# Performance work log

Measured on AMD Instinct MI355X. Metric: run time of the kernel, lower is better.

## Reference

```python
import jax, jax.numpy as jnp
import numpy as np

D_MODEL = 1024
IDX_DIM = 64
SEQ = 4096
D_STATE = 64
EXPAND = 1
HEADDIM = 32
D_CONV = 4
D_INNER = EXPAND * D_MODEL
NHEADS = D_INNER // HEADDIM
CONV_DIM = D_INNER + 2 * D_STATE
D_IN_PROJ = 2 * D_INNER + 2 * D_STATE + NHEADS  # z, xBC, dt


def setup_inputs() -> dict:
    key = jax.random.key(0)
    ks = jax.random.split(key, 8)
    def rn(k, shape, scale=1.0):
        return jax.random.normal(k, shape, jnp.float32) * scale
    return {
        "x": rn(ks[0], (SEQ, D_MODEL)),
        "W_in": rn(ks[1], (D_IN_PROJ, D_MODEL), D_MODEL ** -0.5),
        "conv_w": rn(ks[2], (CONV_DIM, D_CONV), D_CONV ** -0.5),
        "conv_b": jnp.zeros((CONV_DIM,), jnp.float32),
        "dt_bias": rn(ks[3], (NHEADS,)),
        "A_log": jnp.log(jnp.arange(1, NHEADS + 1, dtype=jnp.float32)),
        "D": jnp.ones((NHEADS,), jnp.float32),
        "norm_w": jnp.ones((D_INNER,), jnp.float32),
        "W_out": rn(ks[4], (D_MODEL, D_INNER), D_INNER ** -0.5),
        "W_q": rn(ks[5], (IDX_DIM, D_MODEL), D_MODEL ** -0.5),
        "W_k": rn(ks[6], (IDX_DIM, D_MODEL), D_MODEL ** -0.5),
    }


def _silu(v):
    return v * jax.nn.sigmoid(v)


def _mamba2(x, W_in, conv_w, conv_b, dt_bias, A_log, Dp, norm_w, W_out):
    L = x.shape[0]
    zxbcdt = x @ W_in.T  # [L, D_IN_PROJ]
    z, xBC, dt = jnp.split(zxbcdt, [D_INNER, D_INNER + CONV_DIM], axis=-1)
    # depthwise causal conv1d, kernel D_CONV
    xc = jax.lax.conv_general_dilated(
        xBC.T[None],               # [1, C, L]
        conv_w[:, None, :],        # [C, 1, K]
        (1,), [(D_CONV - 1, 0)], feature_group_count=CONV_DIM)[0].T
    xBC = _silu(xc + conv_b)
    xs, B, C = jnp.split(xBC, [D_INNER, D_INNER + D_STATE], axis=-1)
    xs = xs.reshape(L, NHEADS, HEADDIM)
    dt = jax.nn.softplus(dt + dt_bias)   # [L, H]
    A = -jnp.exp(A_log)                  # [H]

    def step(h, inp):
        x_t, B_t, C_t, dt_t = inp        # [H,P], [N], [N], [H]
        dA = jnp.exp(dt_t * A)           # [H]
        h = h * dA[:, None, None] + (dt_t[:, None] * x_t)[:, :, None] * B_t[None, None, :]
        return h, jnp.einsum('hpn,n->hp', h, C_t)

    h0 = jnp.zeros((NHEADS, HEADDIM, D_STATE), x.dtype)
    _, ys = jax.lax.scan(step, h0, (xs, B, C, dt))  # ys: [L, H, P]
    y = ys + Dp[None, :, None] * xs
    y = y.reshape(L, D_INNER)
    y = y * _silu(z)                                 # gated RMSNorm
    y = y * jax.lax.rsqrt(jnp.mean(y * y, axis=-1, keepdims=True) + 1e-5) * norm_w
    return y @ W_out.T


def reference(x, W_in, conv_w, conv_b, dt_bias, A_log, D, norm_w, W_out, W_q, W_k):
    L = x.shape[0]
    x_mamba = _mamba2(x, W_in, conv_w, conv_b, dt_bias, A_log, D, norm_w, W_out)
    q = x_mamba @ W_q.T                  # [L, IDX_DIM]
    k = x @ W_k.T                        # [L, IDX_DIM]
    scores = jnp.einsum('ti,si->ts', q, k) * (IDX_DIM ** -0.5)
    mask = jnp.tril(jnp.ones((L, L), dtype=bool))
    return jnp.where(mask, scores, -jnp.inf)
```

## Files before the change

kernel.cpp:

```cpp
#include <hip/hip_runtime.h>
#include <math.h>

#define L_SEQ 4096
#define DMODEL 1024
#define DINNER 1024
#define DSTATE 64
#define NH 32
#define HD 32
#define CONVD 1152
#define DPROJ2 2272
#define KOFF 2208
#define QC 128
#define NC 32

#define NEG_FILL (-1e30f)

typedef __attribute__((ext_vector_type(8))) short short8;
typedef __attribute__((ext_vector_type(4))) float f32x4;
typedef unsigned short u16;

__device__ __forceinline__ u16 f2bf(float f) {
  unsigned int u = __float_as_uint(f);
  unsigned int r = (u + 0x7fffu + ((u >> 16) & 1u)) >> 16;
  return (u16)r;
}
__device__ __forceinline__ float bf2f(u16 b) {
  unsigned int u = ((unsigned int)b) << 16;
  return __uint_as_float(u);
}
__device__ __forceinline__ short8 pack8(float4 a, float4 b) {
  short8 v;
  v[0] = (short)f2bf(a.x); v[1] = (short)f2bf(a.y);
  v[2] = (short)f2bf(a.z); v[3] = (short)f2bf(a.w);
  v[4] = (short)f2bf(b.x); v[5] = (short)f2bf(b.y);
  v[6] = (short)f2bf(b.z); v[7] = (short)f2bf(b.w);
  return v;
}

__device__ __forceinline__ void g2l16(const void* g, void* l) {
  __builtin_amdgcn_global_load_lds(
      (const __attribute__((address_space(1))) unsigned int*)g,
      (__attribute__((address_space(3))) unsigned int*)l, 16, 0, 0);
}

#define CAST_N0 (L_SEQ * DMODEL / 8)
#define CAST_N1 (2208 * DMODEL / 8)
#define CAST_N2 (64 * DMODEL / 8)
#define CAST_TOTAL (CAST_N0 + CAST_N1 + 2 * CAST_N2)
#define CAST_BLKS (CAST_TOTAL / 256)
__global__ __launch_bounds__(256) void cast_tr_k(const float* __restrict__ x,
                                                 const float* __restrict__ W_in,
                                                 const float* __restrict__ W_k,
                                                 const float* __restrict__ W_q,
                                                 const float* __restrict__ W_out,
                                                 u16* __restrict__ x_bf,
                                                 u16* __restrict__ Wcat,
                                                 u16* __restrict__ Wq_bf,
                                                 u16* __restrict__ WoutT) {
  __shared__ float tile[64][65];
  int bid = blockIdx.x;
  if (bid < CAST_BLKS) {
    int gid = bid * 256 + threadIdx.x;
    const float* src;
    u16* dst;
    int i;
    if (gid < CAST_N0) { src = x; dst = x_bf; i = gid; }
    else if (gid < CAST_N0 + CAST_N1) { src = W_in; dst = Wcat; i = gid - CAST_N0; }
    else if (gid < CAST_N0 + CAST_N1 + CAST_N2) {
      src = W_k; dst = Wcat + (size_t)2208 * DMODEL; i = gid - CAST_N0 - CAST_N1;
    } else { src = W_q; dst = Wq_bf; i = gid - CAST_N0 - CAST_N1 - CAST_N2; }
    i *= 8;
    float4 f0 = *(const float4*)(src + i);
    float4 f1 = *(const float4*)(src + i + 4);
    *(short8*)(dst + i) = pack8(f0, f1);
    return;
  }
  bid -= CAST_BLKS;
  int bx = bid & 15, by = bid >> 4;
  int tx = threadIdx.x & 63, ty = threadIdx.x >> 6;
#pragma unroll
  for (int k = 0; k < 16; k++) {
    int r = ty + k * 4;
    tile[r][tx] = W_out[(size_t)(by * 64 + r) * 1024 + bx * 64 + tx];
  }
  __syncthreads();
#pragma unroll
  for (int k = 0; k < 16; k++) {
    int r = ty + k * 4;
    WoutT[(size_t)(bx * 64 + r) * 1024 + by * 64 + tx] = f2bf(tile[tx][r]);
  }
}

__global__ __launch_bounds__(256) void wqo_k(const u16* __restrict__ Wq,
                                             const u16* __restrict__ WoutT,
                                             u16* __restrict__ Wqo) {
  const int tid = threadIdx.x;
  const int wave = tid >> 6, lane = tid & 63;
  const int l15 = lane & 15, quad = lane >> 4;
  const int j0 = blockIdx.x * 64;
  f32x4 acc[4] = {};
  for (int kk = 0; kk < 32; kk++) {
    short8 b = *(const short8*)(WoutT + (size_t)(j0 + wave * 16 + l15) * 1024 + kk * 32 + quad * 8);
#pragma unroll
    for (int mi = 0; mi < 4; mi++) {
      short8 a = *(const short8*)(Wq + (size_t)(mi * 16 + l15) * 1024 + kk * 32 + quad * 8);
      acc[mi] = __builtin_amdgcn_mfma_f32_16x16x32_bf16(a, b, acc[mi], 0, 0, 0);
    }
  }
#pragma unroll
  for (int mi = 0; mi < 4; mi++)
#pragma unroll
    for (int r = 0; r < 4; r++) {
      int i = mi * 16 + quad * 4 + r;
      Wqo[(size_t)i * 1024 + j0 + wave * 16 + l15] = f2bf(acc[mi][r]);
    }
}

__global__ __launch_bounds__(256) void gemm128(const u16* __restrict__ A,
                                               const u16* __restrict__ B,
                                               u16* __restrict__ Cbf,
                                               int M, int N, int K) {
  __shared__ u16 As[128 * 32];
  __shared__ u16 Bs[128 * 32];
  const int tid = threadIdx.x;
  const int wave = tid >> 6, lane = tid & 63;
  const int m0 = blockIdx.x * 128, n0 = blockIdx.y * 128;
  const int wm = (wave >> 1) * 64, wn = (wave & 1) * 64;
  const int l15 = lane & 15, quad = lane >> 4;

  const u16* aptr[2];
  const u16* bptr[2];
  char *ldsA[2], *ldsB[2];
#pragma unroll
  for (int b = 0; b < 2; b++) {
    int ch = b * 256 + tid;
    int row = ch >> 2, q = (ch & 3) ^ ((row >> 1) & 3);
    aptr[b] = A + (size_t)(m0 + row) * K + q * 8;
    int bn = min(n0 + row, N - 1);
    bptr[b] = B + (size_t)bn * K + q * 8;
    ldsA[b] = (char*)As + b * 4096 + wave * 1024;
    ldsB[b] = (char*)Bs + b * 4096 + wave * 1024;
  }

  int offA[4], offB[4];
#pragma unroll
  for (int i = 0; i < 4; i++) {
    int ra = wm + i * 16 + l15;
    offA[i] = ra * 32 + (quad ^ ((ra >> 1) & 3)) * 8;
    int rb = wn + i * 16 + l15;
    offB[i] = rb * 32 + (quad ^ ((rb >> 1) & 3)) * 8;
  }

  f32x4 acc[4][4] = {};
  for (int k0 = 0; k0 < K; k0 += 32) {
#pragma unroll
    for (int b = 0; b < 2; b++) g2l16(aptr[b] + k0, ldsA[b]);
#pragma unroll
    for (int b = 0; b < 2; b++) g2l16(bptr[b] + k0, ldsB[b]);
    __builtin_amdgcn_s_waitcnt(0);
    __syncthreads();
    short8 af[4], bfr[4];
#pragma unroll
    for (int i = 0; i < 4; i++) af[i] = *(const short8*)(As + offA[i]);
#pragma unroll
    for (int j = 0; j < 4; j++) bfr[j] = *(const short8*)(Bs + offB[j]);
#pragma unroll
    for (int mi = 0; mi < 4; mi++)
#pragma unroll
      for (int ni = 0; ni < 4; ni++)
        acc[mi][ni] = __builtin_amdgcn_mfma_f32_16x16x32_bf16(af[mi], bfr[ni],
                                                              acc[mi][ni], 0, 0, 0);
    __syncthreads();
  }
#pragma unroll
  for (int mi = 0; mi < 4; mi++)
#pragma unroll
    for (int r = 0; r < 4; r++) {
      int grow = m0 + wm + mi * 16 + quad * 4 + r;
#pragma unroll
      for (int ni = 0; ni < 4; ni++) {
        int gcol = n0 + wn + ni * 16 + l15;
        if (gcol < N) Cbf[(size_t)grow * N + gcol] = f2bf(acc[mi][ni][r]);
      }
    }
}

__global__ __launch_bounds__(256) void splitk64(const u16* __restrict__ A,
                                                const u16* __restrict__ B,
                                                float* __restrict__ P,
                                                int M, int K) {
  __shared__ u16 As[128 * 32];
  __shared__ u16 Bs[64 * 32];
  const int tid = threadIdx.x;
  const int wave = tid >> 6, lane = tid & 63;
  const int m0 = blockIdx.x * 128;
  const int ks = blockIdx.y;
  const int wm = (wave >> 1) * 64, wn = (wave & 1) * 32;
  const int l15 = lane & 15, quad = lane >> 4;

  const int c0 = tid, c1 = 256 + tid;
  const int r0 = c0 >> 2, q0 = (c0 & 3) ^ ((r0 >> 1) & 3);
  const int r1 = c1 >> 2, q1 = (c1 & 3) ^ ((r1 >> 1) & 3);
  const int rb = tid >> 2, qb = (tid & 3) ^ ((rb >> 1) & 3);
  const u16* a0 = A + (size_t)(m0 + r0) * K + q0 * 8;
  const u16* a1 = A + (size_t)(m0 + r1) * K + q1 * 8;
  const u16* bptr = B + (size_t)rb * K + qb * 8;
  char* ldsA0 = (char*)As + wave * 1024;
  char* ldsA1 = (char*)As + 4096 + wave * 1024;
  char* ldsB = (char*)Bs + wave * 1024;

  int offA[4], offB[2];
#pragma unroll
  for (int i = 0; i < 4; i++) {
    int ra = wm + i * 16 + l15;
    offA[i] = ra * 32 + (quad ^ ((ra >> 1) & 3)) * 8;
  }
#pragma unroll
  for (int j = 0; j < 2; j++) {
    int rr = wn + j * 16 + l15;
    offB[j] = rr * 32 + (quad ^ ((rr >> 1) & 3)) * 8;
  }

  f32x4 acc[4][2] = {};
  const int kbeg = ks * 128;
  for (int k0 = kbeg; k0 < kbeg + 128; k0 += 32) {
    g2l16(a0 + k0, ldsA0);
    g2l16(a1 + k0, ldsA1);
    g2l16(bptr + k0, ldsB);
    __builtin_amdgcn_s_waitcnt(0);
    __syncthreads();
    short8 af[4], bfr[2];
#pragma unroll
    for (int i = 0; i < 4; i++) af[i] = *(const short8*)(As + offA[i]);
#pragma unroll
    for (int j = 0; j < 2; j++) bfr[j] = *(const short8*)(Bs + offB[j]);
#pragma unroll
    for (int mi = 0; mi < 4; mi++)
#pragma unroll
      for (int ni = 0; ni < 2; ni++)
        acc[mi][ni] = __builtin_amdgcn_mfma_f32_16x16x32_bf16(af[mi], bfr[ni],
                                                              acc[mi][ni], 0, 0, 0);
    __syncthreads();
  }
  float* Pp = P + (size_t)ks * M * 64;
#pragma unroll
  for (int mi = 0; mi < 4; mi++)
#pragma unroll
    for (int r = 0; r < 4; r++) {
      int grow = m0 + wm + mi * 16 + quad * 4 + r;
#pragma unroll
      for (int ni = 0; ni < 2; ni++)
        Pp[(size_t)grow * 64 + wn + ni * 16 + l15] = acc[mi][ni][r];
    }
}

__global__ __launch_bounds__(256) void reduce8_k(const float* __restrict__ P,
                                                 u16* __restrict__ out, int n) {
  int i = blockIdx.x * 256 + threadIdx.x;
  if (i >= n) return;
  float s = 0.f;
#pragma unroll
  for (int ks = 0; ks < 8; ks++) s += P[(size_t)ks * n + i];
  out[i] = f2bf(s);
}

#define CONV_BLKS (L_SEQ * 144 / 256)
__global__ __launch_bounds__(256) void conv_dt_k(const u16* __restrict__ zx,
                                                 const float* __restrict__ cw,
                                                 const float* __restrict__ cb,
                                                 u16* __restrict__ xbc,
                                                 const float* __restrict__ dt_bias,
                                                 const float* __restrict__ A_log,
                                                 float* __restrict__ dtsp,
                                                 float* __restrict__ aL) {
  if (blockIdx.x < CONV_BLKS) {
    int gid = blockIdx.x * 256 + threadIdx.x;
    int t = gid / 144;
    int c0 = (gid - t * 144) * 8;
    float acc[8];
#pragma unroll
    for (int j = 0; j < 8; j++) acc[j] = cb[c0 + j];
    float wv[8][4];
#pragma unroll
    for (int j = 0; j < 8; j++) {
      float4 w4 = *(const float4*)(cw + (c0 + j) * 4);
      wv[j][0] = w4.x; wv[j][1] = w4.y; wv[j][2] = w4.z; wv[j][3] = w4.w;
    }
#pragma unroll
    for (int k = 0; k < 4; k++) {
      int s = t - 3 + k;
      if (s >= 0) {
        short8 v = *(const short8*)(zx + (size_t)s * DPROJ2 + DINNER + c0);
#pragma unroll
        for (int j = 0; j < 8; j++) acc[j] += bf2f((u16)v[j]) * wv[j][k];
      }
    }
    short8 o;
#pragma unroll
    for (int j = 0; j < 8; j++) o[j] = (short)f2bf(acc[j] / (1.f + expf(-acc[j])));
    *(short8*)(xbc + (size_t)t * CONVD + c0) = o;
    return;
  }
  int w = threadIdx.x >> 6, lane = threadIdx.x & 63;
  int idx = (blockIdx.x - CONV_BLKS) * 4 + w;
  int h = idx & 31, c = idx >> 5;
  float negA = -expf(A_log[h]);
  float bias = dt_bias[h];
  float carry = 0.f;
#pragma unroll
  for (int seg = 0; seg < 2; seg++) {
    int t = c * QC + seg * 64 + lane;
    float xv = bf2f(zx[(size_t)t * DPROJ2 + 2176 + h]) + bias;
    float sp = (xv > 20.f) ? xv : log1pf(expf(xv));
    dtsp[(size_t)t * 32 + h] = sp;
    float v = sp * negA;
#pragma unroll
    for (int off = 1; off < 64; off <<= 1) {
      float u = __shfl_up(v, off, 64);
      if (lane >= off) v += u;
    }
    aL[(size_t)t * 32 + h] = carry + v;
    carry += __shfl(v, 63, 64);
  }
}

__global__ __launch_bounds__(256) void csg_k(const u16* __restrict__ xbc,
                                             const float* __restrict__ dtsp,
                                             const float* __restrict__ aL,
                                             float* __restrict__ S,
                                             float* __restrict__ G) {
  int tid = threadIdx.x;
  const int wave = tid >> 6, lane = tid & 63;
  const int l15 = lane & 15, quad = lane >> 4;
  __shared__ __align__(16) u16 sXs[32 * 136];
  __shared__ __align__(16) u16 sBT[64 * 136];
  __shared__ float scoef[QC];
  if (blockIdx.x < (unsigned)(NC * NH)) {
    int h = blockIdx.x & 31, c = blockIdx.x >> 5;
    if (tid < QC) {
      float aend = aL[(size_t)(c * QC + QC - 1) * 32 + h];
      float a = aL[(size_t)(c * QC + tid) * 32 + h];
      scoef[tid] = expf(aend - a) * dtsp[(size_t)(c * QC + tid) * 32 + h];
    }
    __syncthreads();
    for (int j = tid; j < 32 * QC / 8; j += 256) {
      int s = j & 127, p0 = (j >> 7) * 8;
      short8 v = *(const short8*)(xbc + (size_t)(c * QC + s) * CONVD + h * HD + p0);
      float cf = scoef[s];
#pragma unroll
      for (int e = 0; e < 8; e++) sXs[(p0 + e) * 136 + s] = f2bf(cf * bf2f((u16)v[e]));
    }
    for (int j = tid; j < 64 * QC / 8; j += 256) {
      int s = j & 127, n0 = (j >> 7) * 8;
      short8 v = *(const short8*)(xbc + (size_t)(c * QC + s) * CONVD + DINNER + n0);
#pragma unroll
      for (int e = 0; e < 8; e++) sBT[(n0 + e) * 136 + s] = (u16)v[e];
    }
    __syncthreads();
    f32x4 acc[2] = {};
#pragma unroll
    for (int kk = 0; kk < 4; kk++) {
      short8 b = *(const short8*)(sBT + (wave * 16 + l15) * 136 + kk * 32 + quad * 8);
#pragma unroll
      for (int i = 0; i < 2; i++) {
        short8 a = *(const short8*)(sXs + (i * 16 + l15) * 136 + kk * 32 + quad * 8);
        acc[i] = __builtin_amdgcn_mfma_f32_16x16x32_bf16(a, b, acc[i], 0, 0, 0);
      }
    }
    float* Sb = S + ((size_t)c * 32 + h) * 2048;
#pragma unroll
    for (int i = 0; i < 2; i++)
#pragma unroll
      for (int r = 0; r < 4; r++) {
        int p = i * 16 + quad * 4 + r;
        Sb[p * 64 + wave * 16 + l15] = acc[i][r];
      }
    return;
  }
  int c = blockIdx.x - NC * NH;
  const int wm = (wave >> 1) * 64, wn = (wave & 1) * 64;
  f32x4 acc[4][4] = {};
#pragma unroll
  for (int kk = 0; kk < 2; kk++) {
    short8 a[4], b[4];
#pragma unroll
    for (int i = 0; i < 4; i++) {
      int t = wm + i * 16 + l15;
      a[i] = *(const short8*)(xbc + (size_t)(c * QC + t) * CONVD + DINNER + DSTATE + kk * 32 + quad * 8);
      int s = wn + i * 16 + l15;
      b[i] = *(const short8*)(xbc + (size_t)(c * QC + s) * CONVD + DINNER + kk * 32 + quad * 8);
    }
#pragma unroll
    for (int mi = 0; mi < 4; mi++)
#pragma unroll
      for (int ni = 0; ni < 4; ni++)
        acc[mi][ni] = __builtin_amdgcn_mfma_f32_16x16x32_bf16(a[mi], b[ni],
                                                              acc[mi][ni], 0, 0, 0);
  }
  float* Gb = G + (size_t)c * QC * QC;
#pragma unroll
  for (int mi = 0; mi < 4; mi++)
#pragma unroll
    for (int r = 0; r < 4; r++) {
      int t = wm + mi * 16 + quad * 4 + r;
#pragma unroll
      for (int ni = 0; ni < 4; ni++)
        Gb[(size_t)t * QC + wn + ni * 16 + l15] = acc[mi][ni][r];
    }
}

__global__ __launch_bounds__(256) void state_scan_k(const float* __restrict__ S,
                                                    const float* __restrict__ aL,
                                                    float* __restrict__ Hinit) {
  int idx = blockIdx.x * 256 + threadIdx.x;
  int h = idx >> 11, rem = idx & 2047;
  float E = 0.f;
#pragma unroll
  for (int c = 0; c < NC; c++) {
    size_t o = ((size_t)c * 32 + h) * 2048 + rem;
    Hinit[o] = E;
    float dec = expf(aL[(size_t)(c * QC + QC - 1) * 32 + h]);
    E = E * dec + S[o];
  }
}

__global__ __launch_bounds__(256) void yout_mfma(const u16* __restrict__ xbc,
                                                 const float* __restrict__ dtsp,
                                                 const float* __restrict__ aL,
                                                 const float* __restrict__ G,
                                                 const float* __restrict__ Hinit,
                                                 const float* __restrict__ Dv,
                                                 u16* __restrict__ y) {
  int h = blockIdx.x & 31, c = blockIdx.x >> 5;
  int tid = threadIdx.x;
  __shared__ __align__(16) u16 sXT[32 * 136];
  __shared__ float sa[QC];
  __shared__ float sd[QC];

  if (tid < QC) {
    sa[tid] = aL[(size_t)(c * QC + tid) * 32 + h];
    sd[tid] = dtsp[(size_t)(c * QC + tid) * 32 + h];
  }
  for (int j = tid; j < 32 * QC / 8; j += 256) {
    int t = j & 127, p0 = (j >> 7) * 8;
    short8 v = *(const short8*)(xbc + (size_t)(c * QC + t) * CONVD + h * HD + p0);
#pragma unroll
    for (int e = 0; e < 8; e++) sXT[(p0 + e) * 136 + t] = (u16)v[e];
  }
  __syncthreads();

  const int wave = tid >> 6, lane = tid & 63;
  const int l15 = lane & 15, quad = lane >> 4;
  f32x4 acc1[2][2] = {};
  f32x4 acc2[2][2] = {};

#pragma unroll
  for (int kk = 0; kk < 4; kk++) {
    short8 b[2];
#pragma unroll
    for (int j = 0; j < 2; j++)
      b[j] = *(const short8*)(sXT + (j * 16 + l15) * 136 + kk * 32 + quad * 8);
#pragma unroll
    for (int i = 0; i < 2; i++) {
      int rmax = wave * 32 + i * 16 + 15;
      if (kk * 32 > rmax) continue;
      int m = wave * 32 + i * 16 + l15;
      float am = sa[m];
      const float* Gp = G + (size_t)c * QC * QC + (size_t)m * QC + kk * 32 + quad * 8;
      float4 g0 = *(const float4*)Gp;
      float4 g1 = *(const float4*)(Gp + 4);
      float gv[8] = {g0.x, g0.y, g0.z, g0.w, g1.x, g1.y, g1.z, g1.w};
      int s0 = kk * 32 + quad * 8;
      short8 a;
#pragma unroll
      for (int j2 = 0; j2 < 8; j2++) {
        int s = s0 + j2;
        float w = 0.f;
        if (s <= m) w = expf(am - sa[s]) * sd[s] * gv[j2];
        a[j2] = (short)f2bf(w);
      }
#pragma unroll
      for (int j = 0; j < 2; j++)
        acc1[i][j] = __builtin_amdgcn_mfma_f32_16x16x32_bf16(a, b[j], acc1[i][j], 0, 0, 0);
    }
  }

  const float* Hbase = Hinit + ((size_t)c * 32 + h) * 2048;
#pragma unroll
  for (int kk = 0; kk < 2; kk++) {
    short8 b[2];
#pragma unroll
    for (int j = 0; j < 2; j++) {
      const float* Hp = Hbase + (size_t)(j * 16 + l15) * 64 + kk * 32 + quad * 8;
      b[j] = pack8(*(const float4*)Hp, *(const float4*)(Hp + 4));
    }
#pragma unroll
    for (int i = 0; i < 2; i++) {
      int t = wave * 32 + i * 16 + l15;
      short8 a = *(const short8*)(xbc + (size_t)(c * QC + t) * CONVD + DINNER + DSTATE + kk * 32 + quad * 8);
#pragma unroll
      for (int j = 0; j < 2; j++)
        acc2[i][j] = __builtin_amdgcn_mfma_f32_16x16x32_bf16(a, b[j], acc2[i][j], 0, 0, 0);
    }
  }

  float Dh = Dv[h];
#pragma unroll
  for (int i = 0; i < 2; i++) {
#pragma unroll
    for (int r = 0; r < 4; r++) {
      int t = wave * 32 + i * 16 + quad * 4 + r;
      float et = expf(sa[t]);
#pragma unroll
      for (int j = 0; j < 2; j++) {
        int p = j * 16 + l15;
        float xv = bf2f(sXT[p * 136 + t]);
        float val = acc1[i][j][r] + et * acc2[i][j][r] + Dh * xv;
        y[(size_t)(c * QC + t) * DINNER + h * HD + p] = f2bf(val);
      }
    }
  }
}

__global__ __launch_bounds__(256) void rmsnorm_k(const u16* __restrict__ y1,
                                                 const u16* __restrict__ zx,
                                                 const float* __restrict__ nw,
                                                 u16* __restrict__ y2) {
  int t = blockIdx.x, tid = threadIdx.x;
  int d0 = tid * 4;
  ushort4 yv = *(const ushort4*)(y1 + (size_t)t * DINNER + d0);
  ushort4 zv = *(const ushort4*)(zx + (size_t)t * DPROJ2 + d0);
  float v[4];
  float ss = 0.f;
  u16 ya[4] = {yv.x, yv.y, yv.z, yv.w};
  u16 za[4] = {zv.x, zv.y, zv.z, zv.w};
#pragma unroll
  for (int i = 0; i < 4; i++) {
    float z = bf2f(za[i]);
    float val = bf2f(ya[i]) * (z / (1.f + expf(-z)));
    v[i] = val;
    ss += val * val;
  }
#pragma unroll
  for (int off = 32; off > 0; off >>= 1) ss += __shfl_xor(ss, off, 64);
  __shared__ float red[4];
  int wid = tid >> 6, lane = tid & 63;
  if (lane == 0) red[wid] = ss;
  __syncthreads();
  ss = red[0] + red[1] + red[2] + red[3];
  float scale = rsqrtf(ss * (1.f / 1024.f) + 1e-5f);
  float4 w4 = *(const float4*)(nw + d0);
  float wa[4] = {w4.x, w4.y, w4.z, w4.w};
  ushort4 o;
  o.x = f2bf(v[0] * scale * wa[0]);
  o.y = f2bf(v[1] * scale * wa[1]);
  o.z = f2bf(v[2] * scale * wa[2]);
  o.w = f2bf(v[3] * scale * wa[3]);
  *(ushort4*)(y2 + (size_t)t * DINNER + d0) = o;
}

__global__ __launch_bounds__(256) void scores_mfma(const u16* __restrict__ q,
                                                   const u16* __restrict__ kmat,
                                                   int kstride,
                                                   float* __restrict__ out) {
  const int m0 = blockIdx.y * 128, n0 = blockIdx.x * 128;
  const int tid = threadIdx.x;
  if (n0 > m0 + 127) {
    f32x4 f = {NEG_FILL, NEG_FILL, NEG_FILL, NEG_FILL};
    for (int i = tid; i < 128 * 32; i += 256) {
      int row = i >> 5, c4 = (i & 31) << 2;
      __builtin_nontemporal_store(f, (f32x4*)(out + (size_t)(m0 + row) * L_SEQ + n0 + c4));
    }
    return;
  }
  const int wave = tid >> 6, lane = tid & 63;
  const int wm = (wave >> 1) * 64, wn = (wave & 1) * 64;
  const int l15 = lane & 15, quad = lane >> 4;
  f32x4 acc[4][4] = {};
#pragma unroll
  for (int kk = 0; kk < 2; kk++) {
    short8 a[4], b[4];
#pragma unroll
    for (int i = 0; i < 4; i++) {
      a[i] = *(const short8*)(q + (size_t)(m0 + wm + i * 16 + l15) * 64 + kk * 32 + quad * 8);
      b[i] = *(const short8*)(kmat + (size_t)(n0 + wn + i * 16 + l15) * kstride + kk * 32 + quad * 8);
    }
#pragma unroll
    for (int mi = 0; mi < 4; mi++)
#pragma unroll
      for (int ni = 0; ni < 4; ni++)
        acc[mi][ni] = __builtin_amdgcn_mfma_f32_16x16x32_bf16(a[mi], b[ni],
                                                              acc[mi][ni], 0, 0, 0);
  }
#pragma unroll
  for (int mi = 0; mi < 4; mi++)
#pragma unroll
    for (int r = 0; r < 4; r++) {
      int row = m0 + wm + mi * 16 + quad * 4 + r;
#pragma unroll
      for (int ni = 0; ni < 4; ni++) {
        int col = n0 + wn + ni * 16 + l15;
        float val = (col <= row) ? acc[mi][ni][r] * 0.125f : NEG_FILL;
        __builtin_nontemporal_store(val, out + (size_t)row * L_SEQ + col);
      }
    }
}

extern "C" void kernel_launch(void* const* d_in, const int* in_sizes, int n_in,
                              void* d_out, int out_size, void* d_ws, size_t ws_size,
                              hipStream_t stream) {
  const float* x       = (const float*)d_in[0];
  const float* W_in    = (const float*)d_in[1];
  const float* conv_w  = (const float*)d_in[2];
  const float* conv_b  = (const float*)d_in[3];
  const float* dt_bias = (const float*)d_in[4];
  const float* A_log   = (const float*)d_in[5];
  const float* Dv      = (const float*)d_in[6];
  const float* norm_w  = (const float*)d_in[7];
  const float* W_out   = (const float*)d_in[8];
  const float* W_q     = (const float*)d_in[9];
  const float* W_k     = (const float*)d_in[10];
  float* out = (float*)d_out;

  char* ws = (char*)d_ws;
  size_t off = 0;
  auto alloc = [&](size_t bytes) {
    void* p = (void*)(ws + off);
    off += (bytes + 255) & ~(size_t)255;
    return p;
  };
  u16* zx_bf    = (u16*)alloc((size_t)L_SEQ * DPROJ2 * 2);
  u16* xbc_bf   = (u16*)alloc((size_t)L_SEQ * CONVD * 2);
  float* dtsp   = (float*)alloc((size_t)L_SEQ * NH * 4);
  float* aL     = (float*)alloc((size_t)L_SEQ * NH * 4);
  float* S      = (float*)alloc((size_t)NC * NH * HD * DSTATE * 4);
  float* Hinit  = (float*)alloc((size_t)NC * NH * HD * DSTATE * 4);
  float* G      = (float*)alloc((size_t)NC * QC * QC * 4);
  u16* y1_bf    = (u16*)alloc((size_t)L_SEQ * DINNER * 2);
  u16* y2_bf    = (u16*)alloc((size_t)L_SEQ * DINNER * 2);
  u16* x_bf     = (u16*)alloc((size_t)L_SEQ * DMODEL * 2);
  u16* Wcat_bf  = (u16*)alloc((size_t)DPROJ2 * DMODEL * 2);
  u16* WoutT_bf = (u16*)alloc((size_t)DMODEL * DINNER * 2);
  u16* Wq_bf    = (u16*)alloc((size_t)64 * DMODEL * 2);
  u16* Wqo_bf   = (u16*)alloc((size_t)64 * DINNER * 2);
  u16* q_bf     = (u16*)alloc((size_t)L_SEQ * 64 * 2);
  float* Pq = S;

  cast_tr_k<<<dim3(CAST_BLKS + 256), 256, 0, stream>>>(x, W_in, W_k, W_q, W_out,
                                                       x_bf, Wcat_bf, Wq_bf, WoutT_bf);
  wqo_k<<<dim3(16), 256, 0, stream>>>(Wq_bf, WoutT_bf, Wqo_bf);
  gemm128<<<dim3(L_SEQ / 128, (DPROJ2 + 127) / 128), 256, 0, stream>>>(
      x_bf, Wcat_bf, zx_bf, L_SEQ, DPROJ2, DMODEL);
  conv_dt_k<<<dim3(CONV_BLKS + NC * NH / 4), 256, 0, stream>>>(
      zx_bf, conv_w, conv_b, xbc_bf, dt_bias, A_log, dtsp, aL);
  csg_k<<<dim3(NC * NH + NC), 256, 0, stream>>>(xbc_bf, dtsp, aL, S, G);
  state_scan_k<<<dim3(NH * HD * DSTATE / 256), 256, 0, stream>>>(S, aL, Hinit);
  yout_mfma<<<dim3(NC * NH), 256, 0, stream>>>(xbc_bf, dtsp, aL, G, Hinit, Dv, y1_bf);
  rmsnorm_k<<<dim3(L_SEQ), 256, 0, stream>>>(y1_bf, zx_bf, norm_w, y2_bf);
  splitk64<<<dim3(L_SEQ / 128, 8), 256, 0, stream>>>(y2_bf, Wqo_bf, Pq, L_SEQ, DINNER);
  reduce8_k<<<dim3(L_SEQ * 64 / 256), 256, 0, stream>>>(Pq, q_bf, L_SEQ * 64);
  scores_mfma<<<dim3(32, 32), 256, 0, stream>>>(q_bf, zx_bf + KOFF, DPROJ2, out);
}
```

Measured before the change: 246.0 us.

## Fuse gated RMSNorm into yout and q-projection; widen GEMM K-tile to 64

Removes the separate rmsnorm kernel. The SiLU(z) gate is applied in yout_mfma, which also accumulates per-row sums of squares with shuffles and atomics. norm_w is folded into the precomputed Wqo weights, and the rsqrt scale is applied per row in reduce8_k, since the scale is linear and commutes with the projection. This cuts one kernel launch and a full y read/write round trip, at the cost of atomics and zero-initialising ssq in conv_dt_k. Separately, the main input-projection GEMM now stages a K-tile of 64 with an 8-way XOR swizzle, halving the number of barrier iterations.

```diff
diff --git a/kernel.cpp b/kernel.cpp
--- a/kernel.cpp
+++ b/kernel.cpp
@@ -93,6 +93,7 @@
 
 __global__ __launch_bounds__(256) void wqo_k(const u16* __restrict__ Wq,
                                              const u16* __restrict__ WoutT,
+                                             const float* __restrict__ nw,
                                              u16* __restrict__ Wqo) {
   const int tid = threadIdx.x;
   const int wave = tid >> 6, lane = tid & 63;
@@ -107,12 +108,14 @@
       acc[mi] = __builtin_amdgcn_mfma_f32_16x16x32_bf16(a, b, acc[mi], 0, 0, 0);
     }
   }
+  int col = j0 + wave * 16 + l15;
+  float w = nw[col];
 #pragma unroll
   for (int mi = 0; mi < 4; mi++)
 #pragma unroll
     for (int r = 0; r < 4; r++) {
       int i = mi * 16 + quad * 4 + r;
-      Wqo[(size_t)i * 1024 + j0 + wave * 16 + l15] = f2bf(acc[mi][r]);
+      Wqo[(size_t)i * 1024 + col] = f2bf(acc[mi][r] * w);
     }
 }
 
@@ -120,21 +123,21 @@
                                                const u16* __restrict__ B,
                                                u16* __restrict__ Cbf,
                                                int M, int N, int K) {
-  __shared__ u16 As[128 * 32];
-  __shared__ u16 Bs[128 * 32];
+  __shared__ u16 As[128 * 64];
+  __shared__ u16 Bs[128 * 64];
   const int tid = threadIdx.x;
   const int wave = tid >> 6, lane = tid & 63;
   const int m0 = blockIdx.x * 128, n0 = blockIdx.y * 128;
   const int wm = (wave >> 1) * 64, wn = (wave & 1) * 64;
   const int l15 = lane & 15, quad = lane >> 4;
 
-  const u16* aptr[2];
-  const u16* bptr[2];
-  char *ldsA[2], *ldsB[2];
-#pragma unroll
-  for (int b = 0; b < 2; b++) {
+  const u16* aptr[4];
+  const u16* bptr[4];
+  char *ldsA[4], *ldsB[4];
+#pragma unroll
+  for (int b = 0; b < 4; b++) {
     int ch = b * 256 + tid;
-    int row = ch >> 2, q = (ch & 3) ^ ((row >> 1) & 3);
+    int row = ch >> 3, q = (ch & 7) ^ (row & 7);
     aptr[b] = A + (size_t)(m0 + row) * K + q * 8;
     int bn = min(n0 + row, N - 1);
     bptr[b] = B + (size_t)bn * K + q * 8;
@@ -142,34 +145,39 @@
     ldsB[b] = (char*)Bs + b * 4096 + wave * 1024;
   }
 
-  int offA[4], offB[4];
-#pragma unroll
-  for (int i = 0; i < 4; i++) {
-    int ra = wm + i * 16 + l15;
-    offA[i] = ra * 32 + (quad ^ ((ra >> 1) & 3)) * 8;
-    int rb = wn + i * 16 + l15;
-    offB[i] = rb * 32 + (quad ^ ((rb >> 1) & 3)) * 8;
-  }
+  int offA[2][4], offB[2][4];
+#pragma unroll
+  for (int kk = 0; kk < 2; kk++)
+#pragma unroll
+    for (int i = 0; i < 4; i++) {
+      int ra = wm + i * 16 + l15;
+      offA[kk][i] = ra * 64 + ((kk * 4 + quad) ^ (ra & 7)) * 8;
+      int rb = wn + i * 16 + l15;
+      offB[kk][i] = rb * 64 + ((kk * 4 + quad) ^ (rb & 7)) * 8;
+    }
 
   f32x4 acc[4][4] = {};
-  for (int k0 = 0; k0 < K; k0 += 32) {
-#pragma unroll
-    for (int b = 0; b < 2; b++) g2l16(aptr[b] + k0, ldsA[b]);
-#pragma unroll
-    for (int b = 0; b < 2; b++) g2l16(bptr[b] + k0, ldsB[b]);
+  for (int k0 = 0; k0 < K; k0 += 64) {
+#pragma unroll
+    for (int b = 0; b < 4; b++) g2l16(aptr[b] + k0, ldsA[b]);
+#pragma unroll
+    for (int b = 0; b < 4; b++) g2l16(bptr[b] + k0, ldsB[b]);
     __builtin_amdgcn_s_waitcnt(0);
     __syncthreads();
-    short8 af[4], bfr[4];
-#pragma unroll
-    for (int i = 0; i < 4; i++) af[i] = *(const short8*)(As + offA[i]);
-#pragma unroll
-    for (int j = 0; j < 4; j++) bfr[j] = *(const short8*)(Bs + offB[j]);
-#pragma unroll
-    for (int mi = 0; mi < 4; mi++)
-#pragma unroll
-      for (int ni = 0; ni < 4; ni++)
-        acc[mi][ni] = __builtin_amdgcn_mfma_f32_16x16x32_bf16(af[mi], bfr[ni],
-                                                              acc[mi][ni], 0, 0, 0);
+#pragma unroll
+    for (int kk = 0; kk < 2; kk++) {
+      short8 af[4], bfr[4];
+#pragma unroll
+      for (int i = 0; i < 4; i++) af[i] = *(const short8*)(As + offA[kk][i]);
+#pragma unroll
+      for (int j = 0; j < 4; j++) bfr[j] = *(const short8*)(Bs + offB[kk][j]);
+#pragma unroll
+      for (int mi = 0; mi < 4; mi++)
+#pragma unroll
+        for (int ni = 0; ni < 4; ni++)
+          acc[mi][ni] = __builtin_amdgcn_mfma_f32_16x16x32_bf16(af[mi], bfr[ni],
+                                                                acc[mi][ni], 0, 0, 0);
+    }
     __syncthreads();
   }
 #pragma unroll
@@ -255,13 +263,15 @@
 }
 
 __global__ __launch_bounds__(256) void reduce8_k(const float* __restrict__ P,
+                                                 const float* __restrict__ ssq,
                                                  u16* __restrict__ out, int n) {
   int i = blockIdx.x * 256 + threadIdx.x;
   if (i >= n) return;
   float s = 0.f;
 #pragma unroll
   for (int ks = 0; ks < 8; ks++) s += P[(size_t)ks * n + i];
-  out[i] = f2bf(s);
+  float sc = rsqrtf(ssq[i >> 6] * (1.f / 1024.f) + 1e-5f);
+  out[i] = f2bf(s * sc);
 }
 
 #define CONV_BLKS (L_SEQ * 144 / 256)
@@ -272,7 +282,8 @@
                                                  const float* __restrict__ dt_bias,
                                                  const float* __restrict__ A_log,
                                                  float* __restrict__ dtsp,
-                                                 float* __restrict__ aL) {
+                                                 float* __restrict__ aL,
+                                                 float* __restrict__ ssq) {
   if (blockIdx.x < CONV_BLKS) {
     int gid = blockIdx.x * 256 + threadIdx.x;
     int t = gid / 144;
@@ -301,6 +312,7 @@
     *(short8*)(xbc + (size_t)t * CONVD + c0) = o;
     return;
   }
+  if (threadIdx.x < 16) ssq[(blockIdx.x - CONV_BLKS) * 16 + threadIdx.x] = 0.f;
   int w = threadIdx.x >> 6, lane = threadIdx.x & 63;
   int idx = (blockIdx.x - CONV_BLKS) * 4 + w;
   int h = idx & 31, c = idx >> 5;
@@ -430,6 +442,8 @@
                                                  const float* __restrict__ G,
                                                  const float* __restrict__ Hinit,
                                                  const float* __restrict__ Dv,
+                                                 const u16* __restrict__ zx,
+                                                 float* __restrict__ ssq,
                                                  u16* __restrict__ y) {
   int h = blockIdx.x & 31, c = blockIdx.x >> 5;
   int tid = threadIdx.x;
@@ -511,52 +525,24 @@
     for (int r = 0; r < 4; r++) {
       int t = wave * 32 + i * 16 + quad * 4 + r;
       float et = expf(sa[t]);
+      float part = 0.f;
 #pragma unroll
       for (int j = 0; j < 2; j++) {
         int p = j * 16 + l15;
         float xv = bf2f(sXT[p * 136 + t]);
         float val = acc1[i][j][r] + et * acc2[i][j][r] + Dh * xv;
-        y[(size_t)(c * QC + t) * DINNER + h * HD + p] = f2bf(val);
+        float z = bf2f(zx[(size_t)(c * QC + t) * DPROJ2 + h * HD + p]);
+        float vg = val * (z / (1.f + expf(-z)));
+        part += vg * vg;
+        y[(size_t)(c * QC + t) * DINNER + h * HD + p] = f2bf(vg);
       }
-    }
-  }
-}
-
-__global__ __launch_bounds__(256) void rmsnorm_k(const u16* __restrict__ y1,
-                                                 const u16* __restrict__ zx,
-                                                 const float* __restrict__ nw,
-                                                 u16* __restrict__ y2) {
-  int t = blockIdx.x, tid = threadIdx.x;
-  int d0 = tid * 4;
-  ushort4 yv = *(const ushort4*)(y1 + (size_t)t * DINNER + d0);
-  ushort4 zv = *(const ushort4*)(zx + (size_t)t * DPROJ2 + d0);
-  float v[4];
-  float ss = 0.f;
-  u16 ya[4] = {yv.x, yv.y, yv.z, yv.w};
-  u16 za[4] = {zv.x, zv.y, zv.z, zv.w};
-#pragma unroll
-  for (int i = 0; i < 4; i++) {
-    float z = bf2f(za[i]);
-    float val = bf2f(ya[i]) * (z / (1.f + expf(-z)));
-    v[i] = val;
-    ss += val * val;
-  }
-#pragma unroll
-  for (int off = 32; off > 0; off >>= 1) ss += __shfl_xor(ss, off, 64);
-  __shared__ float red[4];
-  int wid = tid >> 6, lane = tid & 63;
-  if (lane == 0) red[wid] = ss;
-  __syncthreads();
-  ss = red[0] + red[1] + red[2] + red[3];
-  float scale = rsqrtf(ss * (1.f / 1024.f) + 1e-5f);
-  float4 w4 = *(const float4*)(nw + d0);
-  float wa[4] = {w4.x, w4.y, w4.z, w4.w};
-  ushort4 o;
-  o.x = f2bf(v[0] * scale * wa[0]);
-  o.y = f2bf(v[1] * scale * wa[1]);
-  o.z = f2bf(v[2] * scale * wa[2]);
-  o.w = f2bf(v[3] * scale * wa[3]);
-  *(ushort4*)(y2 + (size_t)t * DINNER + d0) = o;
+      part += __shfl_xor(part, 1, 64);
+      part += __shfl_xor(part, 2, 64);
+      part += __shfl_xor(part, 4, 64);
+      part += __shfl_xor(part, 8, 64);
+      if (l15 == 0) atomicAdd(ssq + c * QC + t, part);
+    }
+  }
 }
 
 __global__ __launch_bounds__(256) void scores_mfma(const u16* __restrict__ q,
@@ -636,8 +622,8 @@
   float* S      = (float*)alloc((size_t)NC * NH * HD * DSTATE * 4);
   float* Hinit  = (float*)alloc((size_t)NC * NH * HD * DSTATE * 4);
   float* G      = (float*)alloc((size_t)NC * QC * QC * 4);
+  float* ssq    = (float*)alloc((size_t)L_SEQ * 4);
   u16* y1_bf    = (u16*)alloc((size_t)L_SEQ * DINNER * 2);
-  u16* y2_bf    = (u16*)alloc((size_t)L_SEQ * DINNER * 2);
   u16* x_bf     = (u16*)alloc((size_t)L_SEQ * DMODEL * 2);
   u16* Wcat_bf  = (u16*)alloc((size_t)DPROJ2 * DMODEL * 2);
   u16* WoutT_bf = (u16*)alloc((size_t)DMODEL * DINNER * 2);
@@ -648,16 +634,16 @@
 
   cast_tr_k<<<dim3(CAST_BLKS + 256), 256, 0, stream>>>(x, W_in, W_k, W_q, W_out,
                                                        x_bf, Wcat_bf, Wq_bf, WoutT_bf);
-  wqo_k<<<dim3(16), 256, 0, stream>>>(Wq_bf, WoutT_bf, Wqo_bf);
+  wqo_k<<<dim3(16), 256, 0, stream>>>(Wq_bf, WoutT_bf, norm_w, Wqo_bf);
   gemm128<<<dim3(L_SEQ / 128, (DPROJ2 + 127) / 128), 256, 0, stream>>>(
       x_bf, Wcat_bf, zx_bf, L_SEQ, DPROJ2, DMODEL);
   conv_dt_k<<<dim3(CONV_BLKS + NC * NH / 4), 256, 0, stream>>>(
-      zx_bf, conv_w, conv_b, xbc_bf, dt_bias, A_log, dtsp, aL);
+      zx_bf, conv_w, conv_b, xbc_bf, dt_bias, A_log, dtsp, aL, ssq);
   csg_k<<<dim3(NC * NH + NC), 256, 0, stream>>>(xbc_bf, dtsp, aL, S, G);
   state_scan_k<<<dim3(NH * HD * DSTATE / 256), 256, 0, stream>>>(S, aL, Hinit);
-  yout_mfma<<<dim3(NC * NH), 256, 0, stream>>>(xbc_bf, dtsp, aL, G, Hinit, Dv, y1_bf);
-  rmsnorm_k<<<dim3(L_SEQ), 256, 0, stream>>>(y1_bf, zx_bf, norm_w, y2_bf);
-  splitk64<<<dim3(L_SEQ / 128, 8), 256, 0, stream>>>(y2_bf, Wqo_bf, Pq, L_SEQ, DINNER);
-  reduce8_k<<<dim3(L_SEQ * 64 / 256), 256, 0, stream>>>(Pq, q_bf, L_SEQ * 64);
+  yout_mfma<<<dim3(NC * NH), 256, 0, stream>>>(xbc_bf, dtsp, aL, G, Hinit, Dv,
+                                               zx_bf, ssq, y1_bf);
+  splitk64<<<dim3(L_SEQ / 128, 8), 256, 0, stream>>>(y1_bf, Wqo_bf, Pq, L_SEQ, DINNER);
+  reduce8_k<<<dim3(L_SEQ * 64 / 256), 256, 0, stream>>>(Pq, ssq, q_bf, L_SEQ * 64);
   scores_mfma<<<dim3(32, 32), 256, 0, stream>>>(q_bf, zx_bf + KOFF, DPROJ2, out);
 }
```

Measured after the change: 240.4 us. 1.02x faster.
